# Kernel optimization log

Measured on AMD Instinct MI355X. Metric: run time of the kernel, lower is better.

## Reference

```python
import jax, jax.numpy as jnp
import numpy as np

N = 50000   # nodes
E = 800000  # edges per layer
D = 128     # feature dim
H = 256     # mlp hidden
O = 3       # output dim


def setup_inputs() -> dict:
    key = jax.random.key(0)
    ks = jax.random.split(key, 16)
    def lin(k, fan_out, fan_in):
        s = 1.0 / np.sqrt(fan_in)
        kw, kb = jax.random.split(k)
        return (jax.random.uniform(kw, (fan_out, fan_in), jnp.float32, -s, s),
                jax.random.uniform(kb, (fan_out,), jnp.float32, -s, s))
    x = jax.random.normal(ks[0], (N, D), jnp.float32)
    edge_idx0 = jax.random.randint(ks[1], (2, E), 0, N, dtype=jnp.int64)
    edge_idx1 = jax.random.randint(ks[2], (2, E), 0, N, dtype=jnp.int64)
    Wl1, bl1 = lin(ks[3], D, D)   # SAGE layer1: lin_l (aggregated neighbors, with bias)
    Wr1, _ = lin(ks[4], D, D)     # SAGE layer1: lin_r (root, no bias)
    Wl2, bl2 = lin(ks[5], D, D)
    Wr2, _ = lin(ks[6], D, D)
    Ws, bs = lin(ks[7], D, D)     # skip_fc
    W1, b1 = lin(ks[8], H, D)     # mlp hidden
    W2, b2 = lin(ks[9], O, H)     # mlp out
    return dict(x=x, edge_idx0=edge_idx0, edge_idx1=edge_idx1,
                Wl1=Wl1, bl1=bl1, Wr1=Wr1, Wl2=Wl2, bl2=bl2, Wr2=Wr2,
                Ws=Ws, bs=bs, W1=W1, b1=b1, W2=W2, b2=b2)


def _sage(x, ei, Wl, bl, Wr):
    # PyG SAGEConv with mean aggregation: out = lin_l(mean_j x_j) + lin_r(x_i)
    src, dst = ei[0], ei[1]
    agg = jax.ops.segment_sum(x[src], dst, num_segments=N)          # [N, D] gather-scatter
    cnt = jax.ops.segment_sum(jnp.ones((ei.shape[1],), x.dtype), dst, num_segments=N)
    agg = agg / jnp.maximum(cnt, 1.0)[:, None]
    return agg @ Wl.T + bl + x @ Wr.T


def reference(x, edge_idx0, edge_idx1, Wl1, bl1, Wr1, Wl2, bl2, Wr2,
              Ws, bs, W1, b1, W2, b2):
    inp = x
    h = _sage(x, edge_idx0, Wl1, bl1, Wr1)
    h = _sage(h, edge_idx1, Wl2, bl2, Wr2)
    h = h + (inp @ Ws.T + bs)            # skip connection
    h = jax.nn.relu(h @ W1.T + b1)       # MLP head
    return h @ W2.T + b2                  # [N, 3]
```

## Files before the change

kernel.cpp:

```cpp
#include <hip/hip_runtime.h>
#include <hip/hip_bf16.h>


#define DD 128
#define SB 8
#define CH 4096
typedef unsigned short u16;
typedef __attribute__((ext_vector_type(8))) short short8;
typedef __attribute__((ext_vector_type(4))) float f32x4;

__device__ inline u16 f2bf(float f) {
    __hip_bfloat16 h = __float2bfloat16(f);
    u16 u;
    __builtin_memcpy(&u, &h, 2);
    return u;
}
__device__ inline unsigned pack2(float lo, float hi) {
    return (unsigned)f2bf(lo) | ((unsigned)f2bf(hi) << 16);
}
__device__ inline float bf_lo(unsigned u) { union { unsigned x; float f; } c; c.x = u << 16; return c.f; }
__device__ inline float bf_hi(unsigned u) { union { unsigned x; float f; } c; c.x = u & 0xffff0000u; return c.f; }

struct CastJobs {
    const float4* src[6];
    uint2* dst[6];
    int qstart[7];
};

__global__ __launch_bounds__(256) void hist1_kernel(CastJobs jb,
                                                    const int* __restrict__ dst0, int* __restrict__ h0,
                                                    const int* __restrict__ dst1, int* __restrict__ h1,
                                                    int e0, int e1, int nb, int P) {
    int bx = blockIdx.x;
    int t = threadIdx.x;
    if (bx >= P) {
        if (blockIdx.y == 0) {
            int q = (bx - P) * 256 + t;
            if (q < jb.qstart[6]) {
                int i = 0;
#pragma unroll
                for (int k = 1; k < 6; ++k) if (q >= jb.qstart[k]) i = k;
                int local = q - jb.qstart[i];
                float4 v = jb.src[i][local];
                jb.dst[i][local] = make_uint2(pack2(v.x, v.y), pack2(v.z, v.w));
            }
        }
        return;
    }
    int arr = blockIdx.y;
    const int* dst = arr ? dst1 : dst0;
    int* hist = arr ? h1 : h0;
    int e = arr ? e1 : e0;
    __shared__ int h[256];
    h[t] = 0;
    __syncthreads();
    int base = bx * CH;
    int hi = min(base + CH, e);
    for (int i = base + t; i < hi; i += 256) atomicAdd(&h[dst[i] >> SB], 1);
    __syncthreads();
    if (t < nb) hist[t * P + bx] = h[t];
}

__global__ __launch_bounds__(256) void rowsum_kernel(const int* __restrict__ h0, int* __restrict__ bs0,
                                                     const int* __restrict__ h1, int* __restrict__ bs1,
                                                     int P) {
    int arr = blockIdx.y;
    const int* hist = arr ? h1 : h0;
    int* bs = arr ? bs1 : bs0;
    int b = blockIdx.x;
    __shared__ int s[256];
    int t = threadIdx.x;
    s[t] = (t < P) ? hist[b * P + t] : 0;
    __syncthreads();
    for (int off = 128; off; off >>= 1) {
        if (t < off) s[t] += s[t + off];
        __syncthreads();
    }
    if (t == 0) bs[b] = s[0];
}

__global__ __launch_bounds__(256) void bscan_kernel(const int* __restrict__ bs0, int* __restrict__ bb0, int* __restrict__ rp0, int e0,
                                                    const int* __restrict__ bs1, int* __restrict__ bb1, int* __restrict__ rp1, int e1,
                                                    int nb, int n) {
    int arr = blockIdx.x;
    const int* bsum = arr ? bs1 : bs0;
    int* bb = arr ? bb1 : bb0;
    int* rp = arr ? rp1 : rp0;
    int E = arr ? e1 : e0;
    __shared__ int s[256];
    int t = threadIdx.x;
    int v = (t < nb) ? bsum[t] : 0;
    s[t] = v;
    __syncthreads();
    for (int off = 1; off < 256; off <<= 1) {
        int u = (t >= off) ? s[t - off] : 0;
        __syncthreads();
        s[t] += u;
        __syncthreads();
    }
    if (t < nb) bb[t] = s[t] - v;
    if (t == 0) { bb[nb] = E; rp[n] = E; }
}

__global__ __launch_bounds__(256) void offs_kernel(int* __restrict__ h0, const int* __restrict__ bb0,
                                                   int* __restrict__ h1, const int* __restrict__ bb1,
                                                   int P) {
    int arr = blockIdx.y;
    int* hist = arr ? h1 : h0;
    const int* bb = arr ? bb1 : bb0;
    int b = blockIdx.x;
    __shared__ int s[256];
    int t = threadIdx.x;
    int v = (t < P) ? hist[b * P + t] : 0;
    s[t] = v;
    __syncthreads();
    for (int off = 1; off < 256; off <<= 1) {
        int u = (t >= off) ? s[t - off] : 0;
        __syncthreads();
        s[t] += u;
        __syncthreads();
    }
    if (t < P) hist[b * P + t] = s[t] - v + bb[b];
}

__global__ __launch_bounds__(256) void scatter1_kernel(
    const int* __restrict__ src0, const int* __restrict__ dst0, const int* __restrict__ h0, unsigned* __restrict__ binned0,
    const int* __restrict__ src1, const int* __restrict__ dst1, const int* __restrict__ h1, unsigned* __restrict__ binned1,
    int e0, int e1, int nb, int P) {
    int arr = blockIdx.y;
    const int* src = arr ? src1 : src0;
    const int* dst = arr ? dst1 : dst0;
    const int* hist = arr ? h1 : h0;
    unsigned* binned = arr ? binned1 : binned0;
    int e = arr ? e1 : e0;
    int p = blockIdx.x;
    __shared__ int cnt[256];
    int t = threadIdx.x;
    if (t < nb) cnt[t] = hist[t * P + p];
    __syncthreads();
    int base = p * CH;
    int hi = min(base + CH, e);
    for (int i = base + t; i < hi; i += 256) {
        int d = dst[i];
        int pos = atomicAdd(&cnt[d >> SB], 1);
        binned[pos] = ((unsigned)d << 16) | (unsigned)src[i];
    }
}

__global__ __launch_bounds__(256) void place_kernel(
    const unsigned* __restrict__ binned0, const int* __restrict__ bb0, int* __restrict__ rp0, u16* __restrict__ csr0,
    const unsigned* __restrict__ binned1, const int* __restrict__ bb1, int* __restrict__ rp1, u16* __restrict__ csr1,
    int n, int nb) {
    int arr = blockIdx.y;
    const unsigned* binned = arr ? binned1 : binned0;
    const int* bb = arr ? bb1 : bb0;
    int* rp = arr ? rp1 : rp0;
    u16* csr = arr ? csr1 : csr0;
    int b = blockIdx.x;
    __shared__ int cnt[256];
    __shared__ int s[256];
    int t = threadIdx.x;
    int base = bb[b], end = bb[b + 1];
    cnt[t] = 0;
    __syncthreads();
    for (int i = base + t; i < end; i += 256)
        atomicAdd(&cnt[(binned[i] >> 16) & 255], 1);
    __syncthreads();
    int deg = cnt[t];
    s[t] = deg;
    __syncthreads();
    for (int off = 1; off < 256; off <<= 1) {
        int u = (t >= off) ? s[t - off] : 0;
        __syncthreads();
        s[t] += u;
        __syncthreads();
    }
    int gpos = base + s[t] - deg;
    int node = (b << SB) + t;
    if (node < n) rp[node] = gpos;
    cnt[t] = gpos;
    __syncthreads();
    for (int i = base + t; i < end; i += 256) {
        unsigned pk = binned[i];
        int ld = (pk >> 16) & 255;
        int pos = atomicAdd(&cnt[ld], 1);
        csr[pos] = (u16)(pk & 0xffffu);
    }
}

__global__ __launch_bounds__(256) void agg1_kernel(const u16* __restrict__ G1,
                                                   const u16* __restrict__ csr,
                                                   const int* __restrict__ rp,
                                                   const float* __restrict__ bl1,
                                                   u16* __restrict__ h1, int n) {
    int g = (blockIdx.x * 256 + threadIdx.x) >> 4;
    int lane = threadIdx.x & 15;
    if (g >= n) return;
    int start = rp[g], end = rp[g + 1];
    int d = end - start;
    const uint4* X4 = (const uint4*)G1;
    float acc[8] = {0.f, 0.f, 0.f, 0.f, 0.f, 0.f, 0.f, 0.f};
    int e = start;
    for (; e + 3 < end; e += 4) {
        int s0 = csr[e], s1 = csr[e + 1], s2 = csr[e + 2], s3 = csr[e + 3];
        uint4 v0 = X4[(size_t)s0 * 48 + lane];
        uint4 v1 = X4[(size_t)s1 * 48 + lane];
        uint4 v2 = X4[(size_t)s2 * 48 + lane];
        uint4 v3 = X4[(size_t)s3 * 48 + lane];
        acc[0] += (bf_lo(v0.x) + bf_lo(v1.x)) + (bf_lo(v2.x) + bf_lo(v3.x));
        acc[1] += (bf_hi(v0.x) + bf_hi(v1.x)) + (bf_hi(v2.x) + bf_hi(v3.x));
        acc[2] += (bf_lo(v0.y) + bf_lo(v1.y)) + (bf_lo(v2.y) + bf_lo(v3.y));
        acc[3] += (bf_hi(v0.y) + bf_hi(v1.y)) + (bf_hi(v2.y) + bf_hi(v3.y));
        acc[4] += (bf_lo(v0.z) + bf_lo(v1.z)) + (bf_lo(v2.z) + bf_lo(v3.z));
        acc[5] += (bf_hi(v0.z) + bf_hi(v1.z)) + (bf_hi(v2.z) + bf_hi(v3.z));
        acc[6] += (bf_lo(v0.w) + bf_lo(v1.w)) + (bf_lo(v2.w) + bf_lo(v3.w));
        acc[7] += (bf_hi(v0.w) + bf_hi(v1.w)) + (bf_hi(v2.w) + bf_hi(v3.w));
    }
    for (; e < end; ++e) {
        uint4 v0 = X4[(size_t)csr[e] * 48 + lane];
        acc[0] += bf_lo(v0.x); acc[1] += bf_hi(v0.x);
        acc[2] += bf_lo(v0.y); acc[3] += bf_hi(v0.y);
        acc[4] += bf_lo(v0.z); acc[5] += bf_hi(v0.z);
        acc[6] += bf_lo(v0.w); acc[7] += bf_hi(v0.w);
    }
    float sc = 1.0f / (float)max(d, 1);
    uint4 m = X4[(size_t)g * 48 + 16 + lane];
    const float4* bl = (const float4*)bl1;
    float4 ba = bl[lane * 2], bb = bl[lane * 2 + 1];
    uint4 r;
    r.x = pack2(acc[0] * sc + bf_lo(m.x) + ba.x, acc[1] * sc + bf_hi(m.x) + ba.y);
    r.y = pack2(acc[2] * sc + bf_lo(m.y) + ba.z, acc[3] * sc + bf_hi(m.y) + ba.w);
    r.z = pack2(acc[4] * sc + bf_lo(m.z) + bb.x, acc[5] * sc + bf_hi(m.z) + bb.y);
    r.w = pack2(acc[6] * sc + bf_lo(m.w) + bb.z, acc[7] * sc + bf_hi(m.w) + bb.w);
    ((uint4*)h1)[(size_t)g * 16 + lane] = r;
}

__global__ __launch_bounds__(256) void agg2_kernel(const u16* __restrict__ G2,
                                                   const u16* __restrict__ G1,
                                                   const u16* __restrict__ csr,
                                                   const int* __restrict__ rp,
                                                   const float* __restrict__ bl2,
                                                   const float* __restrict__ bs,
                                                   u16* __restrict__ h3, int n) {
    int g = (blockIdx.x * 256 + threadIdx.x) >> 4;
    int lane = threadIdx.x & 15;
    if (g >= n) return;
    int start = rp[g], end = rp[g + 1];
    int d = end - start;
    const uint4* X4 = (const uint4*)G2;
    float acc[8] = {0.f, 0.f, 0.f, 0.f, 0.f, 0.f, 0.f, 0.f};
    int e = start;
    for (; e + 3 < end; e += 4) {
        int s0 = csr[e], s1 = csr[e + 1], s2 = csr[e + 2], s3 = csr[e + 3];
        uint4 v0 = X4[(size_t)s0 * 32 + lane];
        uint4 v1 = X4[(size_t)s1 * 32 + lane];
        uint4 v2 = X4[(size_t)s2 * 32 + lane];
        uint4 v3 = X4[(size_t)s3 * 32 + lane];
        acc[0] += (bf_lo(v0.x) + bf_lo(v1.x)) + (bf_lo(v2.x) + bf_lo(v3.x));
        acc[1] += (bf_hi(v0.x) + bf_hi(v1.x)) + (bf_hi(v2.x) + bf_hi(v3.x));
        acc[2] += (bf_lo(v0.y) + bf_lo(v1.y)) + (bf_lo(v2.y) + bf_lo(v3.y));
        acc[3] += (bf_hi(v0.y) + bf_hi(v1.y)) + (bf_hi(v2.y) + bf_hi(v3.y));
        acc[4] += (bf_lo(v0.z) + bf_lo(v1.z)) + (bf_lo(v2.z) + bf_lo(v3.z));
        acc[5] += (bf_hi(v0.z) + bf_hi(v1.z)) + (bf_hi(v2.z) + bf_hi(v3.z));
        acc[6] += (bf_lo(v0.w) + bf_lo(v1.w)) + (bf_lo(v2.w) + bf_lo(v3.w));
        acc[7] += (bf_hi(v0.w) + bf_hi(v1.w)) + (bf_hi(v2.w) + bf_hi(v3.w));
    }
    for (; e < end; ++e) {
        uint4 v0 = X4[(size_t)csr[e] * 32 + lane];
        acc[0] += bf_lo(v0.x); acc[1] += bf_hi(v0.x);
        acc[2] += bf_lo(v0.y); acc[3] += bf_hi(v0.y);
        acc[4] += bf_lo(v0.z); acc[5] += bf_hi(v0.z);
        acc[6] += bf_lo(v0.w); acc[7] += bf_hi(v0.w);
    }
    float sc = 1.0f / (float)max(d, 1);
    uint4 m2 = X4[(size_t)g * 32 + 16 + lane];
    uint4 m1 = ((const uint4*)G1)[(size_t)g * 48 + 32 + lane];
    const float4* c2 = (const float4*)bl2;
    const float4* cs = (const float4*)bs;
    float4 ba = c2[lane * 2], bb = c2[lane * 2 + 1];
    float4 sa = cs[lane * 2], sb = cs[lane * 2 + 1];
    uint4 r;
    r.x = pack2(acc[0] * sc + bf_lo(m2.x) + bf_lo(m1.x) + ba.x + sa.x,
                acc[1] * sc + bf_hi(m2.x) + bf_hi(m1.x) + ba.y + sa.y);
    r.y = pack2(acc[2] * sc + bf_lo(m2.y) + bf_lo(m1.y) + ba.z + sa.z,
                acc[3] * sc + bf_hi(m2.y) + bf_hi(m1.y) + ba.w + sa.w);
    r.z = pack2(acc[4] * sc + bf_lo(m2.z) + bf_lo(m1.z) + bb.x + sb.x,
                acc[5] * sc + bf_hi(m2.z) + bf_hi(m1.z) + bb.y + sb.y);
    r.w = pack2(acc[6] * sc + bf_lo(m2.w) + bf_lo(m1.w) + bb.z + sb.z,
                acc[7] * sc + bf_hi(m2.w) + bf_hi(m1.w) + bb.w + sb.w);
    ((uint4*)h3)[(size_t)g * 16 + lane] = r;
}

template <bool F32A>
__global__ __launch_bounds__(256) void mfma_gemm(const void* __restrict__ Av,
                                                 const u16* __restrict__ W,
                                                 u16* __restrict__ C, int M, int NC) {
    __shared__ u16 Bs[32 * 512];
    const int t = threadIdx.x;
    const int colBase = blockIdx.y * 128;
#pragma unroll
    for (int i = 0; i < 8; ++i) {
        int id = t + 256 * i;
        int nrow = id >> 4, cc = id & 15;
        int f = ((nrow >> 4) << 2) | (cc >> 2);
        int dl = ((cc & 3) << 4) | (nrow & 15);
        *(uint4*)&Bs[(f * 64 + dl) * 8] = ((const uint4*)W)[(size_t)(colBase + nrow) * 16 + cc];
    }
    __syncthreads();
    const int w = t >> 6, lane = t & 63, r = lane & 15, half = lane >> 4;
    short8 bf[32];
#pragma unroll
    for (int f = 0; f < 32; ++f)
        bf[f] = *(const short8*)&Bs[(f * 64 + lane) * 8];
    const int nTiles = M >> 4;
    const int nWaves = gridDim.x * 4;
    for (int tile = blockIdx.x * 4 + w; tile < nTiles; tile += nWaves) {
        int rowA = (tile << 4) + r;
        short8 af[4];
        if (F32A) {
            const float4* Arow = (const float4*)Av + (size_t)rowA * 32 + half * 2;
#pragma unroll
            for (int kk = 0; kk < 4; ++kk) {
                float4 a = Arow[kk * 8], b = Arow[kk * 8 + 1];
                uint4 v = make_uint4(pack2(a.x, a.y), pack2(a.z, a.w),
                                     pack2(b.x, b.y), pack2(b.z, b.w));
                af[kk] = *(short8*)&v;
            }
        } else {
            const uint4* Arow = (const uint4*)Av + (size_t)rowA * 16 + half;
#pragma unroll
            for (int kk = 0; kk < 4; ++kk) {
                uint4 v = Arow[kk * 4];
                af[kk] = *(short8*)&v;
            }
        }
        f32x4 acc[8];
#pragma unroll
        for (int i = 0; i < 8; ++i) acc[i] = (f32x4){0.f, 0.f, 0.f, 0.f};
#pragma unroll
        for (int kk = 0; kk < 4; ++kk)
#pragma unroll
            for (int ct = 0; ct < 8; ++ct)
                acc[ct] = __builtin_amdgcn_mfma_f32_16x16x32_bf16(af[kk], bf[ct * 4 + kk], acc[ct], 0, 0, 0);
#pragma unroll
        for (int ct = 0; ct < 8; ++ct) {
            int col = colBase + ct * 16 + r;
#pragma unroll
            for (int reg = 0; reg < 4; ++reg) {
                int row = (tile << 4) + half * 4 + reg;
                C[(size_t)row * NC + col] = f2bf(acc[ct][reg]);
            }
        }
    }
}

__global__ __launch_bounds__(256) void gemm_out_kernel(const u16* __restrict__ h3,
                                                       const u16* __restrict__ W1,
                                                       const float* __restrict__ b1,
                                                       const float* __restrict__ W2,
                                                       const float* __restrict__ b2,
                                                       float* __restrict__ out, int M) {
    __shared__ u16 Bs[64 * 512];
    __shared__ float w2s[3 * 256];
    __shared__ float b1s[256];
    const int t = threadIdx.x;
#pragma unroll
    for (int i = 0; i < 16; ++i) {
        int id = t + 256 * i;
        int nrow = id >> 4, cc = id & 15;
        int f = ((nrow >> 4) << 2) | (cc >> 2);
        int dl = ((cc & 3) << 4) | (nrow & 15);
        *(uint4*)&Bs[(f * 64 + dl) * 8] = ((const uint4*)W1)[(size_t)nrow * 16 + cc];
    }
    for (int i = t; i < 768; i += 256) w2s[i] = W2[i];
    b1s[t] = b1[t];
    __syncthreads();
    const int w = t >> 6, lane = t & 63, r = lane & 15, half = lane >> 4;
    const int nTiles = M >> 4;
    const int nWaves = gridDim.x * 4;
    const u16* bB = &Bs[lane * 8];
    float c0 = b2[0], c1 = b2[1], c2 = b2[2];
    for (int tile = blockIdx.x * 4 + w; tile < nTiles; tile += nWaves) {
        int rowA = (tile << 4) + r;
        const uint4* Arow = (const uint4*)h3 + (size_t)rowA * 16 + half;
        short8 af[4];
#pragma unroll
        for (int kk = 0; kk < 4; ++kk) {
            uint4 v = Arow[kk * 4];
            af[kk] = *(short8*)&v;
        }
        f32x4 acc[16];
#pragma unroll
        for (int i = 0; i < 16; ++i) acc[i] = (f32x4){0.f, 0.f, 0.f, 0.f};
#pragma unroll
        for (int kk = 0; kk < 4; ++kk)
#pragma unroll
            for (int ct = 0; ct < 16; ++ct) {
                short8 bf = *(const short8*)(bB + (ct * 4 + kk) * 512);
                acc[ct] = __builtin_amdgcn_mfma_f32_16x16x32_bf16(af[kk], bf, acc[ct], 0, 0, 0);
            }
        float p[4][3] = {{0.f, 0.f, 0.f}, {0.f, 0.f, 0.f}, {0.f, 0.f, 0.f}, {0.f, 0.f, 0.f}};
#pragma unroll
        for (int ct = 0; ct < 16; ++ct) {
            int col = ct * 16 + r;
            float bv = b1s[col];
            float w0 = w2s[col], w1 = w2s[256 + col], w2v = w2s[512 + col];
#pragma unroll
            for (int reg = 0; reg < 4; ++reg) {
                float h4 = fmaxf(acc[ct][reg] + bv, 0.f);
                p[reg][0] += h4 * w0;
                p[reg][1] += h4 * w1;
                p[reg][2] += h4 * w2v;
            }
        }
#pragma unroll
        for (int m = 1; m < 16; m <<= 1)
#pragma unroll
            for (int reg = 0; reg < 4; ++reg) {
                p[reg][0] += __shfl_xor(p[reg][0], m);
                p[reg][1] += __shfl_xor(p[reg][1], m);
                p[reg][2] += __shfl_xor(p[reg][2], m);
            }
        if (r == 0) {
#pragma unroll
            for (int reg = 0; reg < 4; ++reg) {
                int row = (tile << 4) + half * 4 + reg;
                out[(size_t)row * 3 + 0] = p[reg][0] + c0;
                out[(size_t)row * 3 + 1] = p[reg][1] + c1;
                out[(size_t)row * 3 + 2] = p[reg][2] + c2;
            }
        }
    }
}

extern "C" void kernel_launch(void* const* d_in, const int* in_sizes, int n_in,
                              void* d_out, int out_size, void* d_ws, size_t ws_size,
                              hipStream_t stream) {
    const float* x   = (const float*)d_in[0];
    const int*   ei0 = (const int*)d_in[1];
    const int*   ei1 = (const int*)d_in[2];
    const float* Wl1 = (const float*)d_in[3];
    const float* bl1 = (const float*)d_in[4];
    const float* Wr1 = (const float*)d_in[5];
    const float* Wl2 = (const float*)d_in[6];
    const float* bl2 = (const float*)d_in[7];
    const float* Wr2 = (const float*)d_in[8];
    const float* Wsk = (const float*)d_in[9];
    const float* bsk = (const float*)d_in[10];
    const float* W1  = (const float*)d_in[11];
    const float* b1  = (const float*)d_in[12];
    const float* W2  = (const float*)d_in[13];
    const float* b2  = (const float*)d_in[14];
    float* out = (float*)d_out;

    const int N  = in_sizes[0] / DD;
    const int E0 = in_sizes[1] / 2;
    const int E1 = in_sizes[2] / 2;
    const int H  = in_sizes[12];

    const int* src0 = ei0;      const int* dst0 = ei0 + E0;
    const int* src1 = ei1;      const int* dst1 = ei1 + E1;

    const int nb   = (N + 255) >> SB;
    const int Emax = (E0 > E1) ? E0 : E1;
    const int P    = (Emax + CH - 1) / CH;

    char* wp = (char*)d_ws;
    auto carve = [&](size_t bytes) { char* p = wp; wp += (bytes + 255) & ~(size_t)255; return p; };
    u16* G1   = (u16*)carve((size_t)N * 384 * 2);
    u16* G2   = (u16*)carve((size_t)N * 256 * 2);
    u16* h1h  = (u16*)carve((size_t)N * DD * 2);
    u16* h3h  = (u16*)carve((size_t)N * DD * 2);
    u16* wc1  = (u16*)carve((size_t)384 * DD * 2);
    u16* wc2  = (u16*)carve((size_t)256 * DD * 2);
    u16* w1h  = (u16*)carve((size_t)H * DD * 2);
    int* rp0  = (int*)carve((size_t)(N + 1) * 4);
    int* rp1  = (int*)carve((size_t)(N + 1) * 4);
    u16* csr0 = (u16*)carve((size_t)E0 * 2);
    u16* csr1 = (u16*)carve((size_t)E1 * 2);
    unsigned* binned0 = (unsigned*)carve((size_t)E0 * 4);
    unsigned* binned1 = (unsigned*)carve((size_t)E1 * 4);
    int* hist1_0 = (int*)carve((size_t)nb * P * 4);
    int* hist1_1 = (int*)carve((size_t)nb * P * 4);
    int* bsum0 = (int*)carve((size_t)nb * 4);
    int* bsum1 = (int*)carve((size_t)nb * 4);
    int* bb0 = (int*)carve((size_t)(nb + 1) * 4);
    int* bb1 = (int*)carve((size_t)(nb + 1) * 4);

    CastJobs jb;
    const float* srcs[6] = {Wl1, Wr1, Wsk, Wl2, Wr2, W1};
    u16* dsts[6] = {wc1, wc1 + 128 * DD, wc1 + 256 * DD, wc2, wc2 + 128 * DD, w1h};
    int  cnts[6] = {DD * DD, DD * DD, DD * DD, DD * DD, DD * DD, H * DD};
    int q = 0;
    for (int i = 0; i < 6; ++i) {
        jb.src[i] = (const float4*)srcs[i];
        jb.dst[i] = (uint2*)dsts[i];
        jb.qstart[i] = q;
        q += cnts[i] / 4;
    }
    jb.qstart[6] = q;
    const int CB = (q + 255) / 256;

    const int gAgg = (N * 16 + 255) / 256;

    hist1_kernel<<<dim3(P + CB, 2), 256, 0, stream>>>(jb, dst0, hist1_0, dst1, hist1_1, E0, E1, nb, P);
    rowsum_kernel<<<dim3(nb, 2), 256, 0, stream>>>(hist1_0, bsum0, hist1_1, bsum1, P);
    bscan_kernel<<<2, 256, 0, stream>>>(bsum0, bb0, rp0, E0, bsum1, bb1, rp1, E1, nb, N);
    offs_kernel<<<dim3(nb, 2), 256, 0, stream>>>(hist1_0, bb0, hist1_1, bb1, P);
    scatter1_kernel<<<dim3(P, 2), 256, 0, stream>>>(src0, dst0, hist1_0, binned0,
                                                    src1, dst1, hist1_1, binned1, E0, E1, nb, P);
    place_kernel<<<dim3(nb, 2), 256, 0, stream>>>(binned0, bb0, rp0, csr0,
                                                  binned1, bb1, rp1, csr1, N, nb);

    mfma_gemm<true><<<dim3(320, 3), 256, 0, stream>>>(x, wc1, G1, N, 384);
    agg1_kernel<<<gAgg, 256, 0, stream>>>(G1, csr0, rp0, bl1, h1h, N);
    mfma_gemm<false><<<dim3(320, 2), 256, 0, stream>>>(h1h, wc2, G2, N, 256);
    agg2_kernel<<<gAgg, 256, 0, stream>>>(G2, G1, csr1, rp1, bl2, bsk, h3h, N);
    gemm_out_kernel<<<512, 256, 0, stream>>>(h3h, w1h, b1, W2, b2, out, N);
}
```

Measured before the change: 253.2 us.

## Split gather features into column quarters pinned to XCDs for L2 locality

The GEMM outputs for the neighbour features are stored as four 32-column slabs (one per quarter of the feature dim). Aggregation blocks are mapped so each XCD pair works on a single quarter, which shrinks each XCD's gather working set (N×32 bf16) enough to fit in its L2. Downstream GEMMs read the quartered layout for A. The x fp32→bf16 cast moves into the cast pre-pass. The cost is more gather instructions per edge at 4-byte width, an extra pass over x, and a dependence on the XCD round-robin block assignment.

```diff
diff --git a/kernel.cpp b/kernel.cpp
--- a/kernel.cpp
+++ b/kernel.cpp
@@ -22,9 +22,9 @@
 __device__ inline float bf_hi(unsigned u) { union { unsigned x; float f; } c; c.x = u & 0xffff0000u; return c.f; }
 
 struct CastJobs {
-    const float4* src[6];
-    uint2* dst[6];
-    int qstart[7];
+    const float4* src[7];
+    uint2* dst[7];
+    int qstart[8];
 };
 
 __global__ __launch_bounds__(256) void hist1_kernel(CastJobs jb,
@@ -36,10 +36,10 @@
     if (bx >= P) {
         if (blockIdx.y == 0) {
             int q = (bx - P) * 256 + t;
-            if (q < jb.qstart[6]) {
+            if (q < jb.qstart[7]) {
                 int i = 0;
 #pragma unroll
-                for (int k = 1; k < 6; ++k) if (q >= jb.qstart[k]) i = k;
+                for (int k = 1; k < 7; ++k) if (q >= jb.qstart[k]) i = k;
                 int local = q - jb.qstart[i];
                 float4 v = jb.src[i][local];
                 jb.dst[i][local] = make_uint2(pack2(v.x, v.y), pack2(v.z, v.w));
@@ -188,116 +188,118 @@
     }
 }
 
-__global__ __launch_bounds__(256) void agg1_kernel(const u16* __restrict__ G1,
+__global__ __launch_bounds__(256) void agg1_kernel(const u16* __restrict__ G1Lq,
+                                                   const u16* __restrict__ G1M,
                                                    const u16* __restrict__ csr,
                                                    const int* __restrict__ rp,
                                                    const float* __restrict__ bl1,
-                                                   u16* __restrict__ h1, int n) {
-    int g = (blockIdx.x * 256 + threadIdx.x) >> 4;
-    int lane = threadIdx.x & 15;
+                                                   u16* __restrict__ h1q, int n) {
+    int xcd = blockIdx.x & 7;
+    int j = blockIdx.x >> 3;
+    int q = xcd & 3;
+    int nbk = j * 2 + (xcd >> 2);
+    int t = threadIdx.x;
+    int g = nbk * 16 + (t >> 4);
+    int lane = t & 15;
     if (g >= n) return;
     int start = rp[g], end = rp[g + 1];
     int d = end - start;
-    const uint4* X4 = (const uint4*)G1;
-    float acc[8] = {0.f, 0.f, 0.f, 0.f, 0.f, 0.f, 0.f, 0.f};
+    const unsigned* GL = (const unsigned*)G1Lq + (size_t)q * n * 16;
+    float a0 = 0.f, a1 = 0.f;
     int e = start;
+    for (; e + 7 < end; e += 8) {
+        int s0 = csr[e], s1 = csr[e + 1], s2 = csr[e + 2], s3 = csr[e + 3];
+        int s4 = csr[e + 4], s5 = csr[e + 5], s6 = csr[e + 6], s7 = csr[e + 7];
+        unsigned v0 = GL[s0 * 16 + lane], v1 = GL[s1 * 16 + lane];
+        unsigned v2 = GL[s2 * 16 + lane], v3 = GL[s3 * 16 + lane];
+        unsigned v4 = GL[s4 * 16 + lane], v5 = GL[s5 * 16 + lane];
+        unsigned v6 = GL[s6 * 16 + lane], v7 = GL[s7 * 16 + lane];
+        a0 += ((bf_lo(v0) + bf_lo(v1)) + (bf_lo(v2) + bf_lo(v3)))
+            + ((bf_lo(v4) + bf_lo(v5)) + (bf_lo(v6) + bf_lo(v7)));
+        a1 += ((bf_hi(v0) + bf_hi(v1)) + (bf_hi(v2) + bf_hi(v3)))
+            + ((bf_hi(v4) + bf_hi(v5)) + (bf_hi(v6) + bf_hi(v7)));
+    }
     for (; e + 3 < end; e += 4) {
         int s0 = csr[e], s1 = csr[e + 1], s2 = csr[e + 2], s3 = csr[e + 3];
-        uint4 v0 = X4[(size_t)s0 * 48 + lane];
-        uint4 v1 = X4[(size_t)s1 * 48 + lane];
-        uint4 v2 = X4[(size_t)s2 * 48 + lane];
-        uint4 v3 = X4[(size_t)s3 * 48 + lane];
-        acc[0] += (bf_lo(v0.x) + bf_lo(v1.x)) + (bf_lo(v2.x) + bf_lo(v3.x));
-        acc[1] += (bf_hi(v0.x) + bf_hi(v1.x)) + (bf_hi(v2.x) + bf_hi(v3.x));
-        acc[2] += (bf_lo(v0.y) + bf_lo(v1.y)) + (bf_lo(v2.y) + bf_lo(v3.y));
-        acc[3] += (bf_hi(v0.y) + bf_hi(v1.y)) + (bf_hi(v2.y) + bf_hi(v3.y));
-        acc[4] += (bf_lo(v0.z) + bf_lo(v1.z)) + (bf_lo(v2.z) + bf_lo(v3.z));
-        acc[5] += (bf_hi(v0.z) + bf_hi(v1.z)) + (bf_hi(v2.z) + bf_hi(v3.z));
-        acc[6] += (bf_lo(v0.w) + bf_lo(v1.w)) + (bf_lo(v2.w) + bf_lo(v3.w));
-        acc[7] += (bf_hi(v0.w) + bf_hi(v1.w)) + (bf_hi(v2.w) + bf_hi(v3.w));
+        unsigned v0 = GL[s0 * 16 + lane], v1 = GL[s1 * 16 + lane];
+        unsigned v2 = GL[s2 * 16 + lane], v3 = GL[s3 * 16 + lane];
+        a0 += (bf_lo(v0) + bf_lo(v1)) + (bf_lo(v2) + bf_lo(v3));
+        a1 += (bf_hi(v0) + bf_hi(v1)) + (bf_hi(v2) + bf_hi(v3));
     }
     for (; e < end; ++e) {
-        uint4 v0 = X4[(size_t)csr[e] * 48 + lane];
-        acc[0] += bf_lo(v0.x); acc[1] += bf_hi(v0.x);
-        acc[2] += bf_lo(v0.y); acc[3] += bf_hi(v0.y);
-        acc[4] += bf_lo(v0.z); acc[5] += bf_hi(v0.z);
-        acc[6] += bf_lo(v0.w); acc[7] += bf_hi(v0.w);
+        unsigned v0 = GL[csr[e] * 16 + lane];
+        a0 += bf_lo(v0); a1 += bf_hi(v0);
     }
     float sc = 1.0f / (float)max(d, 1);
-    uint4 m = X4[(size_t)g * 48 + 16 + lane];
-    const float4* bl = (const float4*)bl1;
-    float4 ba = bl[lane * 2], bb = bl[lane * 2 + 1];
-    uint4 r;
-    r.x = pack2(acc[0] * sc + bf_lo(m.x) + ba.x, acc[1] * sc + bf_hi(m.x) + ba.y);
-    r.y = pack2(acc[2] * sc + bf_lo(m.y) + ba.z, acc[3] * sc + bf_hi(m.y) + ba.w);
-    r.z = pack2(acc[4] * sc + bf_lo(m.z) + bb.x, acc[5] * sc + bf_hi(m.z) + bb.y);
-    r.w = pack2(acc[6] * sc + bf_lo(m.w) + bb.z, acc[7] * sc + bf_hi(m.w) + bb.w);
-    ((uint4*)h1)[(size_t)g * 16 + lane] = r;
-}
-
-__global__ __launch_bounds__(256) void agg2_kernel(const u16* __restrict__ G2,
-                                                   const u16* __restrict__ G1,
+    unsigned m = ((const unsigned*)G1M)[(size_t)g * 64 + q * 16 + lane];
+    float2 bb = ((const float2*)bl1)[q * 16 + lane];
+    ((unsigned*)h1q)[(size_t)q * n * 16 + g * 16 + lane] =
+        pack2(a0 * sc + bf_lo(m) + bb.x, a1 * sc + bf_hi(m) + bb.y);
+}
+
+__global__ __launch_bounds__(256) void agg2_kernel(const u16* __restrict__ G2Lq,
+                                                   const u16* __restrict__ G2R,
+                                                   const u16* __restrict__ G1R,
                                                    const u16* __restrict__ csr,
                                                    const int* __restrict__ rp,
                                                    const float* __restrict__ bl2,
                                                    const float* __restrict__ bs,
-                                                   u16* __restrict__ h3, int n) {
-    int g = (blockIdx.x * 256 + threadIdx.x) >> 4;
-    int lane = threadIdx.x & 15;
+                                                   u16* __restrict__ h3q, int n) {
+    int xcd = blockIdx.x & 7;
+    int j = blockIdx.x >> 3;
+    int q = xcd & 3;
+    int nbk = j * 2 + (xcd >> 2);
+    int t = threadIdx.x;
+    int g = nbk * 16 + (t >> 4);
+    int lane = t & 15;
     if (g >= n) return;
     int start = rp[g], end = rp[g + 1];
     int d = end - start;
-    const uint4* X4 = (const uint4*)G2;
-    float acc[8] = {0.f, 0.f, 0.f, 0.f, 0.f, 0.f, 0.f, 0.f};
+    const unsigned* GL = (const unsigned*)G2Lq + (size_t)q * n * 16;
+    float a0 = 0.f, a1 = 0.f;
     int e = start;
+    for (; e + 7 < end; e += 8) {
+        int s0 = csr[e], s1 = csr[e + 1], s2 = csr[e + 2], s3 = csr[e + 3];
+        int s4 = csr[e + 4], s5 = csr[e + 5], s6 = csr[e + 6], s7 = csr[e + 7];
+        unsigned v0 = GL[s0 * 16 + lane], v1 = GL[s1 * 16 + lane];
+        unsigned v2 = GL[s2 * 16 + lane], v3 = GL[s3 * 16 + lane];
+        unsigned v4 = GL[s4 * 16 + lane], v5 = GL[s5 * 16 + lane];
+        unsigned v6 = GL[s6 * 16 + lane], v7 = GL[s7 * 16 + lane];
+        a0 += ((bf_lo(v0) + bf_lo(v1)) + (bf_lo(v2) + bf_lo(v3)))
+            + ((bf_lo(v4) + bf_lo(v5)) + (bf_lo(v6) + bf_lo(v7)));
+        a1 += ((bf_hi(v0) + bf_hi(v1)) + (bf_hi(v2) + bf_hi(v3)))
+            + ((bf_hi(v4) + bf_hi(v5)) + (bf_hi(v6) + bf_hi(v7)));
+    }
     for (; e + 3 < end; e += 4) {
         int s0 = csr[e], s1 = csr[e + 1], s2 = csr[e + 2], s3 = csr[e + 3];
-        uint4 v0 = X4[(size_t)s0 * 32 + lane];
-        uint4 v1 = X4[(size_t)s1 * 32 + lane];
-        uint4 v2 = X4[(size_t)s2 * 32 + lane];
-        uint4 v3 = X4[(size_t)s3 * 32 + lane];
-        acc[0] += (bf_lo(v0.x) + bf_lo(v1.x)) + (bf_lo(v2.x) + bf_lo(v3.x));
-        acc[1] += (bf_hi(v0.x) + bf_hi(v1.x)) + (bf_hi(v2.x) + bf_hi(v3.x));
-        acc[2] += (bf_lo(v0.y) + bf_lo(v1.y)) + (bf_lo(v2.y) + bf_lo(v3.y));
-        acc[3] += (bf_hi(v0.y) + bf_hi(v1.y)) + (bf_hi(v2.y) + bf_hi(v3.y));
-        acc[4] += (bf_lo(v0.z) + bf_lo(v1.z)) + (bf_lo(v2.z) + bf_lo(v3.z));
-        acc[5] += (bf_hi(v0.z) + bf_hi(v1.z)) + (bf_hi(v2.z) + bf_hi(v3.z));
-        acc[6] += (bf_lo(v0.w) + bf_lo(v1.w)) + (bf_lo(v2.w) + bf_lo(v3.w));
-        acc[7] += (bf_hi(v0.w) + bf_hi(v1.w)) + (bf_hi(v2.w) + bf_hi(v3.w));
+        unsigned v0 = GL[s0 * 16 + lane], v1 = GL[s1 * 16 + lane];
+        unsigned v2 = GL[s2 * 16 + lane], v3 = GL[s3 * 16 + lane];
+        a0 += (bf_lo(v0) + bf_lo(v1)) + (bf_lo(v2) + bf_lo(v3));
+        a1 += (bf_hi(v0) + bf_hi(v1)) + (bf_hi(v2) + bf_hi(v3));
     }
     for (; e < end; ++e) {
-        uint4 v0 = X4[(size_t)csr[e] * 32 + lane];
-        acc[0] += bf_lo(v0.x); acc[1] += bf_hi(v0.x);
-        acc[2] += bf_lo(v0.y); acc[3] += bf_hi(v0.y);
-        acc[4] += bf_lo(v0.z); acc[5] += bf_hi(v0.z);
-        acc[6] += bf_lo(v0.w); acc[7] += bf_hi(v0.w);
+        unsigned v0 = GL[csr[e] * 16 + lane];
+        a0 += bf_lo(v0); a1 += bf_hi(v0);
     }
     float sc = 1.0f / (float)max(d, 1);
-    uint4 m2 = X4[(size_t)g * 32 + 16 + lane];
-    uint4 m1 = ((const uint4*)G1)[(size_t)g * 48 + 32 + lane];
-    const float4* c2 = (const float4*)bl2;
-    const float4* cs = (const float4*)bs;
-    float4 ba = c2[lane * 2], bb = c2[lane * 2 + 1];
-    float4 sa = cs[lane * 2], sb = cs[lane * 2 + 1];
-    uint4 r;
-    r.x = pack2(acc[0] * sc + bf_lo(m2.x) + bf_lo(m1.x) + ba.x + sa.x,
-                acc[1] * sc + bf_hi(m2.x) + bf_hi(m1.x) + ba.y + sa.y);
-    r.y = pack2(acc[2] * sc + bf_lo(m2.y) + bf_lo(m1.y) + ba.z + sa.z,
-                acc[3] * sc + bf_hi(m2.y) + bf_hi(m1.y) + ba.w + sa.w);
-    r.z = pack2(acc[4] * sc + bf_lo(m2.z) + bf_lo(m1.z) + bb.x + sb.x,
-                acc[5] * sc + bf_hi(m2.z) + bf_hi(m1.z) + bb.y + sb.y);
-    r.w = pack2(acc[6] * sc + bf_lo(m2.w) + bf_lo(m1.w) + bb.z + sb.z,
-                acc[7] * sc + bf_hi(m2.w) + bf_hi(m1.w) + bb.w + sb.w);
-    ((uint4*)h3)[(size_t)g * 16 + lane] = r;
-}
-
-template <bool F32A>
-__global__ __launch_bounds__(256) void mfma_gemm(const void* __restrict__ Av,
+    unsigned m2 = ((const unsigned*)G2R)[(size_t)g * 64 + q * 16 + lane];
+    unsigned m1 = ((const unsigned*)G1R)[(size_t)g * 64 + q * 16 + lane];
+    float2 cb = ((const float2*)bl2)[q * 16 + lane];
+    float2 sb = ((const float2*)bs)[q * 16 + lane];
+    ((unsigned*)h3q)[(size_t)q * n * 16 + g * 16 + lane] =
+        pack2(a0 * sc + bf_lo(m2) + bf_lo(m1) + cb.x + sb.x,
+              a1 * sc + bf_hi(m2) + bf_hi(m1) + cb.y + sb.y);
+}
+
+template <bool QA>
+__global__ __launch_bounds__(256) void mfma_gemm(const u16* __restrict__ A,
                                                  const u16* __restrict__ W,
-                                                 u16* __restrict__ C, int M, int NC) {
+                                                 u16* __restrict__ Cq,
+                                                 u16* __restrict__ Crow, int M) {
     __shared__ u16 Bs[32 * 512];
     const int t = threadIdx.x;
-    const int colBase = blockIdx.y * 128;
+    const int y = blockIdx.y;
+    const int colBase = y * 128;
 #pragma unroll
     for (int i = 0; i < 8; ++i) {
         int id = t + 256 * i;
@@ -314,25 +316,15 @@
         bf[f] = *(const short8*)&Bs[(f * 64 + lane) * 8];
     const int nTiles = M >> 4;
     const int nWaves = gridDim.x * 4;
+    const uint4* A4 = (const uint4*)A;
     for (int tile = blockIdx.x * 4 + w; tile < nTiles; tile += nWaves) {
         int rowA = (tile << 4) + r;
         short8 af[4];
-        if (F32A) {
-            const float4* Arow = (const float4*)Av + (size_t)rowA * 32 + half * 2;
-#pragma unroll
-            for (int kk = 0; kk < 4; ++kk) {
-                float4 a = Arow[kk * 8], b = Arow[kk * 8 + 1];
-                uint4 v = make_uint4(pack2(a.x, a.y), pack2(a.z, a.w),
-                                     pack2(b.x, b.y), pack2(b.z, b.w));
-                af[kk] = *(short8*)&v;
-            }
-        } else {
-            const uint4* Arow = (const uint4*)Av + (size_t)rowA * 16 + half;
-#pragma unroll
-            for (int kk = 0; kk < 4; ++kk) {
-                uint4 v = Arow[kk * 4];
-                af[kk] = *(short8*)&v;
-            }
+#pragma unroll
+        for (int kk = 0; kk < 4; ++kk) {
+            uint4 v = QA ? A4[(size_t)kk * M * 4 + (size_t)rowA * 4 + half]
+                         : A4[(size_t)rowA * 16 + half + kk * 4];
+            af[kk] = *(short8*)&v;
         }
         f32x4 acc[8];
 #pragma unroll
@@ -342,19 +334,33 @@
 #pragma unroll
             for (int ct = 0; ct < 8; ++ct)
                 acc[ct] = __builtin_amdgcn_mfma_f32_16x16x32_bf16(af[kk], bf[ct * 4 + kk], acc[ct], 0, 0, 0);
-#pragma unroll
-        for (int ct = 0; ct < 8; ++ct) {
-            int col = colBase + ct * 16 + r;
-#pragma unroll
-            for (int reg = 0; reg < 4; ++reg) {
-                int row = (tile << 4) + half * 4 + reg;
-                C[(size_t)row * NC + col] = f2bf(acc[ct][reg]);
+        if (y == 0) {
+#pragma unroll
+            for (int ct = 0; ct < 8; ++ct) {
+                int col = ct * 16 + r;
+                int qq = col >> 5, ww = col & 31;
+#pragma unroll
+                for (int reg = 0; reg < 4; ++reg) {
+                    int row = (tile << 4) + half * 4 + reg;
+                    Cq[((size_t)qq * M + row) * 32 + ww] = f2bf(acc[ct][reg]);
+                }
+            }
+        } else {
+            u16* Cr = Crow + (size_t)(y - 1) * M * 128;
+#pragma unroll
+            for (int ct = 0; ct < 8; ++ct) {
+                int col = ct * 16 + r;
+#pragma unroll
+                for (int reg = 0; reg < 4; ++reg) {
+                    int row = (tile << 4) + half * 4 + reg;
+                    Cr[(size_t)row * 128 + col] = f2bf(acc[ct][reg]);
+                }
             }
         }
     }
 }
 
-__global__ __launch_bounds__(256) void gemm_out_kernel(const u16* __restrict__ h3,
+__global__ __launch_bounds__(256) void gemm_out_kernel(const u16* __restrict__ h3q,
                                                        const u16* __restrict__ W1,
                                                        const float* __restrict__ b1,
                                                        const float* __restrict__ W2,
@@ -379,14 +385,14 @@
     const int nTiles = M >> 4;
     const int nWaves = gridDim.x * 4;
     const u16* bB = &Bs[lane * 8];
+    const uint4* A4 = (const uint4*)h3q;
     float c0 = b2[0], c1 = b2[1], c2 = b2[2];
     for (int tile = blockIdx.x * 4 + w; tile < nTiles; tile += nWaves) {
         int rowA = (tile << 4) + r;
-        const uint4* Arow = (const uint4*)h3 + (size_t)rowA * 16 + half;
         short8 af[4];
 #pragma unroll
         for (int kk = 0; kk < 4; ++kk) {
-            uint4 v = Arow[kk * 4];
+            uint4 v = A4[(size_t)kk * M * 4 + (size_t)rowA * 4 + half];
             af[kk] = *(short8*)&v;
         }
         f32x4 acc[16];
@@ -467,10 +473,13 @@
 
     char* wp = (char*)d_ws;
     auto carve = [&](size_t bytes) { char* p = wp; wp += (bytes + 255) & ~(size_t)255; return p; };
-    u16* G1   = (u16*)carve((size_t)N * 384 * 2);
-    u16* G2   = (u16*)carve((size_t)N * 256 * 2);
-    u16* h1h  = (u16*)carve((size_t)N * DD * 2);
-    u16* h3h  = (u16*)carve((size_t)N * DD * 2);
+    u16* xbf  = (u16*)carve((size_t)N * 128 * 2);
+    u16* G1Lq = (u16*)carve((size_t)N * 128 * 2);
+    u16* G1MR = (u16*)carve((size_t)N * 256 * 2);
+    u16* G2Lq = (u16*)carve((size_t)N * 128 * 2);
+    u16* G2R  = (u16*)carve((size_t)N * 128 * 2);
+    u16* h1q  = (u16*)carve((size_t)N * 128 * 2);
+    u16* h3q  = (u16*)carve((size_t)N * 128 * 2);
     u16* wc1  = (u16*)carve((size_t)384 * DD * 2);
     u16* wc2  = (u16*)carve((size_t)256 * DD * 2);
     u16* w1h  = (u16*)carve((size_t)H * DD * 2);
@@ -487,21 +496,26 @@
     int* bb0 = (int*)carve((size_t)(nb + 1) * 4);
     int* bb1 = (int*)carve((size_t)(nb + 1) * 4);
 
+    u16* G1M = G1MR;
+    u16* G1R = G1MR + (size_t)N * 128;
+
     CastJobs jb;
-    const float* srcs[6] = {Wl1, Wr1, Wsk, Wl2, Wr2, W1};
-    u16* dsts[6] = {wc1, wc1 + 128 * DD, wc1 + 256 * DD, wc2, wc2 + 128 * DD, w1h};
-    int  cnts[6] = {DD * DD, DD * DD, DD * DD, DD * DD, DD * DD, H * DD};
+    const float* srcs[7] = {Wl1, Wr1, Wsk, Wl2, Wr2, W1, x};
+    u16* dsts[7] = {wc1, wc1 + 128 * DD, wc1 + 256 * DD, wc2, wc2 + 128 * DD, w1h, xbf};
+    int  cnts[7] = {DD * DD, DD * DD, DD * DD, DD * DD, DD * DD, H * DD, N * DD};
     int q = 0;
-    for (int i = 0; i < 6; ++i) {
+    for (int i = 0; i < 7; ++i) {
         jb.src[i] = (const float4*)srcs[i];
         jb.dst[i] = (uint2*)dsts[i];
         jb.qstart[i] = q;
         q += cnts[i] / 4;
     }
-    jb.qstart[6] = q;
+    jb.qstart[7] = q;
     const int CB = (q + 255) / 256;
 
-    const int gAgg = (N * 16 + 255) / 256;
+    const int NBK = (N + 15) / 16;
+    const int perX = (NBK + 1) / 2;
+    const int gAggQ = 8 * perX;
 
     hist1_kernel<<<dim3(P + CB, 2), 256, 0, stream>>>(jb, dst0, hist1_0, dst1, hist1_1, E0, E1, nb, P);
     rowsum_kernel<<<dim3(nb, 2), 256, 0, stream>>>(hist1_0, bsum0, hist1_1, bsum1, P);
@@ -512,9 +526,9 @@
     place_kernel<<<dim3(nb, 2), 256, 0, stream>>>(binned0, bb0, rp0, csr0,
                                                   binned1, bb1, rp1, csr1, N, nb);
 
-    mfma_gemm<true><<<dim3(320, 3), 256, 0, stream>>>(x, wc1, G1, N, 384);
-    agg1_kernel<<<gAgg, 256, 0, stream>>>(G1, csr0, rp0, bl1, h1h, N);
-    mfma_gemm<false><<<dim3(320, 2), 256, 0, stream>>>(h1h, wc2, G2, N, 256);
-    agg2_kernel<<<gAgg, 256, 0, stream>>>(G2, G1, csr1, rp1, bl2, bsk, h3h, N);
-    gemm_out_kernel<<<512, 256, 0, stream>>>(h3h, w1h, b1, W2, b2, out, N);
-}
+    mfma_gemm<false><<<dim3(320, 3), 256, 0, stream>>>(xbf, wc1, G1Lq, G1M, N);
+    agg1_kernel<<<gAggQ, 256, 0, stream>>>(G1Lq, G1M, csr0, rp0, bl1, h1q, N);
+    mfma_gemm<true><<<dim3(320, 2), 256, 0, stream>>>(h1q, wc2, G2Lq, G2R, N);
+    agg2_kernel<<<gAggQ, 256, 0, stream>>>(G2Lq, G2R, G1R, csr1, rp1, bl2, bsk, h3q, N);
+    gemm_out_kernel<<<512, 256, 0, stream>>>(h3q, w1h, b1, W2, b2, out, N);
+}
```

Measured after the change: 270.9 us. 7.0% more time.
